# Kernel optimization log

Hardware: AMD Instinct MI355X
Metric: run time of the kernel (lower is better)

The kernel has to match this reference:

```python
import jax, jax.numpy as jnp
import numpy as np

B = 4096
H = 8            # history_len
P = 13           # num_piece_types
D = 256          # d_model
NUM_TC = 8
BOARD_DIM = H * P + 1   # 105
META_DIM = H + H + 4 + 8  # 28


def setup_inputs() -> dict:
    key = jax.random.key(0)
    ks = jax.random.split(key, 16)
    inp = {
        "board_history": jax.random.randint(ks[0], (B, H, 64), 0, P, dtype=jnp.int64),
        "time_history": jax.random.uniform(ks[1], (B, H), dtype=jnp.float32),
        "rep_flags": jax.random.uniform(ks[2], (B, H), dtype=jnp.float32),
        "castling": jax.random.uniform(ks[3], (B, 4), dtype=jnp.float32),
        "ep_mask": jax.random.uniform(ks[4], (B, 64), dtype=jnp.float32),
        "scalars": jax.random.normal(ks[5], (B, 8), dtype=jnp.float32),
        "tc_cat": jax.random.randint(ks[6], (B,), 0, NUM_TC, dtype=jnp.int64),
        # learned params (torch Linear weight is (out,in); we store (in,out))
        "W_board": 0.02 * jax.random.normal(ks[7], (BOARD_DIM, D), dtype=jnp.float32),
        "W_meta": 0.001 * jax.random.normal(ks[8], (META_DIM, D), dtype=jnp.float32),
        "square_emb": jax.random.normal(ks[9], (64, D), dtype=jnp.float32),
        "square_scale": jnp.ones((64, D), dtype=jnp.float32),
        "square_bias": jnp.zeros((64, D), dtype=jnp.float32),
        "tc_table": jax.random.normal(ks[10], (NUM_TC, D), dtype=jnp.float32),
    }
    return inp


def reference(board_history, time_history, rep_flags, castling, ep_mask, scalars,
              tc_cat, W_board, W_meta, square_emb, square_scale, square_bias, tc_table):
    b = board_history.shape[0]
    # one-hot(piece_code, 13): (B, H, 64, P) -> (B, 64, H*P)
    oh = jax.nn.one_hot(board_history, P, dtype=jnp.float32)
    board_oh = jnp.transpose(oh, (0, 2, 1, 3)).reshape(b, 64, H * P)
    # board input = [one-hot history, ep flag]  -> (B, 64, 105)
    board_in = jnp.concatenate([board_oh, ep_mask[..., None]], axis=-1)
    # meta features are identical across squares; project once per batch row
    meta = jnp.concatenate([time_history, rep_flags, castling, scalars], axis=-1)  # (B, 28)
    meta_vec = meta @ W_meta  # (B, D)
    x = jnp.einsum("bsf,fd->bsd", board_in, W_board) + meta_vec[:, None, :]
    x = x + square_emb[None, :, :]
    x = x * square_scale + square_bias
    x = x + tc_table[tc_cat][:, None, :]
    return x
```

## Files before the change

### kernel.cpp

```cpp
#include <hip/hip_runtime.h>
#include <hip/hip_bf16.h>


#define D 256
#define HD 8
#define PD 13

__global__ __launch_bounds__(256) void encoder_kernel(
    const int*   __restrict__ board,
    const float* __restrict__ time_h,
    const float* __restrict__ rep,
    const float* __restrict__ castl,
    const float* __restrict__ ep,
    const float* __restrict__ scal,
    const int*   __restrict__ tc_cat,
    const float* __restrict__ Wb,
    const float* __restrict__ Wm,
    const float* __restrict__ emb,
    const float* __restrict__ sscale,
    const float* __restrict__ sbias,
    const float* __restrict__ tc_tab,
    float*       __restrict__ out)
{
    const int b   = blockIdx.x;
    const int tid = threadIdx.x;

    __shared__ float s_meta[28];
    __shared__ float s_mv[D];
    __shared__ float s_tc[D];
    __shared__ int   s_board[HD * 64];
    __shared__ float s_ep[64];

    if (tid < 8)        s_meta[tid]      = time_h[b * 8 + tid];
    else if (tid < 16)  s_meta[tid]      = rep[b * 8 + (tid - 8)];
    else if (tid < 20)  s_meta[tid]      = castl[b * 4 + (tid - 16)];
    else if (tid < 28)  s_meta[tid]      = scal[b * 8 + (tid - 20)];

    s_board[tid]       = board[b * 512 + tid];
    s_board[tid + 256] = board[b * 512 + 256 + tid];
    if (tid < 64) s_ep[tid] = ep[b * 64 + tid];

    const int tcc = tc_cat[b];
    s_tc[tid] = tc_tab[tcc * D + tid];
    __syncthreads();

    float mv = 0.0f;
    #pragma unroll
    for (int f = 0; f < 28; ++f)
        mv = fmaf(s_meta[f], Wm[f * D + tid], mv);
    s_mv[tid] = mv;
    __syncthreads();

    const int wave = tid >> 6;
    const int lane = tid & 63;
    const int d    = lane * 4;

    const float4 mv4  = *(const float4*)(&s_mv[d]);
    const float4 tc4  = *(const float4*)(&s_tc[d]);
    const float4 w104 = *(const float4*)(&Wb[104 * D + d]);

    for (int s = wave; s < 64; s += 4) {
        float4 acc = mv4;
        #pragma unroll
        for (int h = 0; h < HD; ++h) {
            const int p = s_board[h * 64 + s];
            const float4 w = *(const float4*)(&Wb[(h * PD + p) * D + d]);
            acc.x += w.x; acc.y += w.y; acc.z += w.z; acc.w += w.w;
        }
        const float epv = s_ep[s];
        acc.x = fmaf(epv, w104.x, acc.x);
        acc.y = fmaf(epv, w104.y, acc.y);
        acc.z = fmaf(epv, w104.z, acc.z);
        acc.w = fmaf(epv, w104.w, acc.w);

        const float4 e  = *(const float4*)(&emb[s * D + d]);
        const float4 sc = *(const float4*)(&sscale[s * D + d]);
        const float4 bi = *(const float4*)(&sbias[s * D + d]);

        float4 x;
        x.x = fmaf(acc.x + e.x, sc.x, bi.x) + tc4.x;
        x.y = fmaf(acc.y + e.y, sc.y, bi.y) + tc4.y;
        x.z = fmaf(acc.z + e.z, sc.z, bi.z) + tc4.z;
        x.w = fmaf(acc.w + e.w, sc.w, bi.w) + tc4.w;

        *(float4*)(&out[(size_t)b * 64 * D + s * D + d]) = x;
    }
}

extern "C" void kernel_launch(void* const* d_in, const int* in_sizes, int n_in,
                              void* d_out, int out_size, void* d_ws, size_t ws_size,
                              hipStream_t stream) {
    const int*   board  = (const int*)  d_in[0];
    const float* time_h = (const float*)d_in[1];
    const float* rep    = (const float*)d_in[2];
    const float* castl  = (const float*)d_in[3];
    const float* ep     = (const float*)d_in[4];
    const float* scal   = (const float*)d_in[5];
    const int*   tc_cat = (const int*)  d_in[6];
    const float* Wb     = (const float*)d_in[7];
    const float* Wm     = (const float*)d_in[8];
    const float* emb    = (const float*)d_in[9];
    const float* sscale = (const float*)d_in[10];
    const float* sbias  = (const float*)d_in[11];
    const float* tc_tab = (const float*)d_in[12];
    float* out = (float*)d_out;

    const int B = in_sizes[6];
    encoder_kernel<<<B, 256, 0, stream>>>(board, time_h, rep, castl, ep, scal,
                                          tc_cat, Wb, Wm, emb, sscale, sbias,
                                          tc_tab, out);
}
```

Measured before the change: 417.0 us.

## Stage bf16-packed board weights in LDS and process eight batch rows per block

Each block now converts the full 105x256 board weight matrix to bf16 and stages it in shared memory. It then loops over eight batch rows, gathering one-hot weight rows from LDS instead of global memory. Precomputed byte offsets replace piece indices, and the meta projection is computed per lane as float4. The goal is to cut global/L2 gather traffic and amortize setup, at the cost of bf16 rounding on weights (a precision loss), about 53KB of LDS per block that limits occupancy, and only 512 blocks.

Measured after the change: 370.9 us. 11.1% less time.

```diff
diff --git a/kernel.cpp b/kernel.cpp
--- a/kernel.cpp
+++ b/kernel.cpp
@@ -5,6 +5,18 @@
 #define D 256
 #define HD 8
 #define PD 13
+#define NB 8
+#define WB_ROWS 105
+#define WB_ELEMS (WB_ROWS * D)
+#define WB_F4    (WB_ELEMS / 4)
+
+__device__ __forceinline__ unsigned short f2bf(float f) {
+    unsigned int u = __float_as_uint(f);
+    unsigned int r = (u + 0x7fffu + ((u >> 16) & 1u)) >> 16;
+    return (unsigned short)r;
+}
+__device__ __forceinline__ float bf_lo(unsigned int u) { return __uint_as_float(u << 16); }
+__device__ __forceinline__ float bf_hi(unsigned int u) { return __uint_as_float(u & 0xffff0000u); }
 
 __global__ __launch_bounds__(256) void encoder_kernel(
     const int*   __restrict__ board,
@@ -20,70 +32,100 @@
     const float* __restrict__ sscale,
     const float* __restrict__ sbias,
     const float* __restrict__ tc_tab,
-    float*       __restrict__ out)
+    float*       __restrict__ out,
+    int Btot)
 {
-    const int b   = blockIdx.x;
-    const int tid = threadIdx.x;
+    __shared__ __align__(16) unsigned short sWb[WB_ELEMS];
+    __shared__ int   s_off[HD * 64];
+    __shared__ float s_ep[64];
+    __shared__ float s_meta[28];
 
-    __shared__ float s_meta[28];
-    __shared__ float s_mv[D];
-    __shared__ float s_tc[D];
-    __shared__ int   s_board[HD * 64];
-    __shared__ float s_ep[64];
-
-    if (tid < 8)        s_meta[tid]      = time_h[b * 8 + tid];
-    else if (tid < 16)  s_meta[tid]      = rep[b * 8 + (tid - 8)];
-    else if (tid < 20)  s_meta[tid]      = castl[b * 4 + (tid - 16)];
-    else if (tid < 28)  s_meta[tid]      = scal[b * 8 + (tid - 20)];
-
-    s_board[tid]       = board[b * 512 + tid];
-    s_board[tid + 256] = board[b * 512 + 256 + tid];
-    if (tid < 64) s_ep[tid] = ep[b * 64 + tid];
-
-    const int tcc = tc_cat[b];
-    s_tc[tid] = tc_tab[tcc * D + tid];
-    __syncthreads();
-
-    float mv = 0.0f;
-    #pragma unroll
-    for (int f = 0; f < 28; ++f)
-        mv = fmaf(s_meta[f], Wm[f * D + tid], mv);
-    s_mv[tid] = mv;
-    __syncthreads();
-
+    const int tid  = threadIdx.x;
     const int wave = tid >> 6;
     const int lane = tid & 63;
     const int d    = lane * 4;
 
-    const float4 mv4  = *(const float4*)(&s_mv[d]);
-    const float4 tc4  = *(const float4*)(&s_tc[d]);
+    for (int i = tid; i < WB_F4; i += 256) {
+        const float4 w = *(const float4*)(Wb + i * 4);
+        uint2 pk;
+        pk.x = (unsigned int)f2bf(w.x) | ((unsigned int)f2bf(w.y) << 16);
+        pk.y = (unsigned int)f2bf(w.z) | ((unsigned int)f2bf(w.w) << 16);
+        *(uint2*)(&sWb[i * 4]) = pk;
+    }
+
     const float4 w104 = *(const float4*)(&Wb[104 * D + d]);
 
-    for (int s = wave; s < 64; s += 4) {
-        float4 acc = mv4;
+    const int b0 = blockIdx.x * NB;
+    const int nb = min(NB, Btot - b0);
+
+    for (int bi = 0; bi < nb; ++bi) {
+        const int b = b0 + bi;
+
+        __syncthreads();
+
+        {
+            int e = tid;
+            #pragma unroll
+            for (int r = 0; r < 2; ++r, e += 256) {
+                const int p = board[b * 512 + e];
+                s_off[e] = ((e >> 6) * PD + p) * (D * 2);
+            }
+        }
+        if (tid < 64) s_ep[tid] = ep[b * 64 + tid];
+        if (tid < 8)        s_meta[tid] = time_h[b * 8 + tid];
+        else if (tid < 16)  s_meta[tid] = rep[b * 8 + (tid - 8)];
+        else if (tid < 20)  s_meta[tid] = castl[b * 4 + (tid - 16)];
+        else if (tid < 28)  s_meta[tid] = scal[b * 8 + (tid - 20)];
+
+        __syncthreads();
+
+        float4 mv = make_float4(0.f, 0.f, 0.f, 0.f);
         #pragma unroll
-        for (int h = 0; h < HD; ++h) {
-            const int p = s_board[h * 64 + s];
-            const float4 w = *(const float4*)(&Wb[(h * PD + p) * D + d]);
-            acc.x += w.x; acc.y += w.y; acc.z += w.z; acc.w += w.w;
+        for (int f = 0; f < 28; ++f) {
+            const float  m = s_meta[f];
+            const float4 w = *(const float4*)(&Wm[f * D + d]);
+            mv.x = fmaf(m, w.x, mv.x);
+            mv.y = fmaf(m, w.y, mv.y);
+            mv.z = fmaf(m, w.z, mv.z);
+            mv.w = fmaf(m, w.w, mv.w);
         }
-        const float epv = s_ep[s];
-        acc.x = fmaf(epv, w104.x, acc.x);
-        acc.y = fmaf(epv, w104.y, acc.y);
-        acc.z = fmaf(epv, w104.z, acc.z);
-        acc.w = fmaf(epv, w104.w, acc.w);
+        const int tcc = tc_cat[b];
+        const float4 tc4 = *(const float4*)(&tc_tab[tcc * D + d]);
 
-        const float4 e  = *(const float4*)(&emb[s * D + d]);
-        const float4 sc = *(const float4*)(&sscale[s * D + d]);
-        const float4 bi = *(const float4*)(&sbias[s * D + d]);
+        const size_t outb = (size_t)b * 64 * D;
+        const char* wb_base = (const char*)sWb + (size_t)lane * 8;
 
-        float4 x;
-        x.x = fmaf(acc.x + e.x, sc.x, bi.x) + tc4.x;
-        x.y = fmaf(acc.y + e.y, sc.y, bi.y) + tc4.y;
-        x.z = fmaf(acc.z + e.z, sc.z, bi.z) + tc4.z;
-        x.w = fmaf(acc.w + e.w, sc.w, bi.w) + tc4.w;
+        #pragma unroll 4
+        for (int i = 0; i < 16; ++i) {
+            const int s = wave * 16 + i;
+            float4 acc = mv;
+            #pragma unroll
+            for (int h = 0; h < HD; ++h) {
+                const int ro = s_off[h * 64 + s];
+                const uint2 u = *(const uint2*)(wb_base + ro);
+                acc.x += bf_lo(u.x);
+                acc.y += bf_hi(u.x);
+                acc.z += bf_lo(u.y);
+                acc.w += bf_hi(u.y);
+            }
+            const float epv = s_ep[s];
+            acc.x = fmaf(epv, w104.x, acc.x);
+            acc.y = fmaf(epv, w104.y, acc.y);
+            acc.z = fmaf(epv, w104.z, acc.z);
+            acc.w = fmaf(epv, w104.w, acc.w);
 
-        *(float4*)(&out[(size_t)b * 64 * D + s * D + d]) = x;
+            const float4 e  = *(const float4*)(&emb[s * D + d]);
+            const float4 sc = *(const float4*)(&sscale[s * D + d]);
+            const float4 bi4 = *(const float4*)(&sbias[s * D + d]);
+
+            float4 x;
+            x.x = fmaf(acc.x + e.x, sc.x, bi4.x) + tc4.x;
+            x.y = fmaf(acc.y + e.y, sc.y, bi4.y) + tc4.y;
+            x.z = fmaf(acc.z + e.z, sc.z, bi4.z) + tc4.z;
+            x.w = fmaf(acc.w + e.w, sc.w, bi4.w) + tc4.w;
+
+            *(float4*)(&out[outb + s * D + d]) = x;
+        }
     }
 }
 
@@ -106,7 +148,8 @@
     float* out = (float*)d_out;
 
     const int B = in_sizes[6];
-    encoder_kernel<<<B, 256, 0, stream>>>(board, time_h, rep, castl, ep, scal,
-                                          tc_cat, Wb, Wm, emb, sscale, sbias,
-                                          tc_tab, out);
+    const int grid = (B + NB - 1) / NB;
+    encoder_kernel<<<grid, 256, 0, stream>>>(board, time_h, rep, castl, ep, scal,
+                                             tc_cat, Wb, Wm, emb, sscale, sbias,
+                                             tc_tab, out, B);
 }
```
